# Performance work log

Hardware: AMD Instinct MI355X
Metric: run time of the kernel (lower is better)

The kernel has to match this reference:

```python
import jax, jax.numpy as jnp
import numpy as np
import math

OUT = 7   # output_size
SR = 2    # sampling_ratio


def _roi_align(feat, rois5, scale):
    """torchvision roi_align (aligned=False) for all rois against one FPN level.
    feat: [B,C,H,W], rois5: [N,5] = (batch_idx, x1, y1, x2, y2). Returns [N,C,OUT,OUT]."""
    B, C, H, W = feat.shape
    b = rois5[:, 0].astype(jnp.int32)
    x1 = rois5[:, 1] * scale
    y1 = rois5[:, 2] * scale
    x2 = rois5[:, 3] * scale
    y2 = rois5[:, 4] * scale
    rw = jnp.maximum(x2 - x1, 1.0)
    rh = jnp.maximum(y2 - y1, 1.0)
    gh = OUT * SR  # sampling grid: ph*SR+iy, sample at (g+0.5)*bin/SR from roi start
    gw = OUT * SR
    ys = y1[:, None] + (jnp.arange(gh, dtype=feat.dtype) + 0.5)[None, :] * (rh / gh)[:, None]  # [N,gh]
    xs = x1[:, None] + (jnp.arange(gw, dtype=feat.dtype) + 0.5)[None, :] * (rw / gw)[:, None]  # [N,gw]
    # torchvision bilinear_interpolate: out-of-range (< -1 or > size) -> 0, else clamp
    vy = (ys >= -1.0) & (ys <= H)
    vx = (xs >= -1.0) & (xs <= W)
    y = jnp.clip(ys, 0.0, H - 1)
    x = jnp.clip(xs, 0.0, W - 1)
    y0f = jnp.floor(y)
    x0f = jnp.floor(x)
    y0 = y0f.astype(jnp.int32)
    x0 = x0f.astype(jnp.int32)
    y1i = jnp.minimum(y0 + 1, H - 1)
    x1i = jnp.minimum(x0 + 1, W - 1)
    ly = y - y0f; hy = 1.0 - ly
    lx = x - x0f; hx = 1.0 - lx
    fT = jnp.transpose(feat, (0, 2, 3, 1))  # [B,H,W,C]

    def gather(yi, xi):
        return fT[b[:, None, None], yi[:, :, None], xi[:, None, :]]  # [N,gh,gw,C]

    w00 = (hy[:, :, None] * hx[:, None, :])[..., None]
    w01 = (hy[:, :, None] * lx[:, None, :])[..., None]
    w10 = (ly[:, :, None] * hx[:, None, :])[..., None]
    w11 = (ly[:, :, None] * lx[:, None, :])[..., None]
    val = (gather(y0, x0) * w00 + gather(y0, x1i) * w01
           + gather(y1i, x0) * w10 + gather(y1i, x1i) * w11)
    val = val * (vy[:, :, None] & vx[:, None, :])[..., None].astype(feat.dtype)
    # average SRxSR samples per output bin -> [N,OUT,OUT,C] -> [N,C,OUT,OUT]
    val = val.reshape(val.shape[0], OUT, SR, OUT, SR, C).mean(axis=(2, 4))
    return jnp.transpose(val, (0, 3, 1, 2))


def setup_inputs() -> dict:
    key = jax.random.key(0)
    ks = jax.random.split(key, 6)
    feat0 = jax.random.normal(ks[0], (2, 256, 200, 200), jnp.float32)
    feat1 = jax.random.normal(ks[1], (2, 256, 100, 100), jnp.float32)
    feat2 = jax.random.normal(ks[2], (2, 256, 50, 50), jnp.float32)
    feat3 = jax.random.normal(ks[3], (2, 256, 25, 25), jnp.float32)
    B, N = 2, 512
    xy1 = jax.random.uniform(ks[4], (B, N, 2), jnp.float32, 0.0, 700.0)
    wh = jax.random.uniform(ks[5], (B, N, 2), jnp.float32, 16.0, 320.0)
    xy2 = jnp.minimum(xy1 + wh, 799.0)
    rois = jnp.concatenate([xy1, xy2], axis=-1)  # [B,N,4] = (x1,y1,x2,y2)
    return {"feat0": feat0, "feat1": feat1, "feat2": feat2, "feat3": feat3,
            "rois": rois, "image_h": 800, "image_w": 800}


def reference(feat0, feat1, feat2, feat3, rois, image_h, image_w):
    feats = [feat0, feat1, feat2, feat3]
    B, N = rois.shape[:2]
    # _convert_to_roi_format: prepend batch index column
    bcol = jnp.repeat(jnp.arange(B, dtype=rois.dtype), N)[:, None]
    rois5 = jnp.concatenate([bcol, rois.reshape(-1, 4)], axis=1)  # [B*N,5]
    # _setup_scales / _get_scales: pow-2-rounded ratio of feature H to image H (static)
    scales = [2.0 ** round(math.log2(f.shape[2] / float(image_h))) for f in feats]
    lvl_min = -math.log2(scales[0])   # 2
    lvl_max = -math.log2(scales[-1])  # 5
    # FPN level routing: k = floor(4 + log2(sqrt(area)/224)), clamped
    area = (rois5[:, 4] - rois5[:, 2]) * (rois5[:, 3] - rois5[:, 1])
    k = jnp.floor(4.0 + jnp.log2(jnp.sqrt(area) / 224.0))
    k = jnp.clip(k, lvl_min, lvl_max) - lvl_min  # in {0,1,2,3}
    out = jnp.zeros((B * N, feats[0].shape[1], OUT, OUT), feats[0].dtype)
    for lvl, (f, s) in enumerate(zip(feats, scales)):
        pooled = _roi_align(f, rois5, s)
        out = jnp.where((k == lvl)[:, None, None, None], pooled, out)
    return out
```

## Files before the change

### kernel.cpp

```cpp
#include <hip/hip_runtime.h>

#define OUTS 7
#define SR 2
#define GRIDW 14
#define NS 196
#define NCH 256
#define NROI 1024
#define NBIN 49

#define L0_OFF 0
#define L1_OFF 20480000
#define L2_OFF 25600000
#define L3_OFF 26880000
#define WS_ELEMS 27200000

static __device__ __forceinline__ unsigned short f2bf(float f) {
    unsigned u = __builtin_bit_cast(unsigned, f);
    u += 0x7fffu + ((u >> 16) & 1u);
    return (unsigned short)(u >> 16);
}

static __device__ __forceinline__ float bfhi(unsigned u) {
    return __builtin_bit_cast(float, u & 0xffff0000u);
}
static __device__ __forceinline__ float bflo(unsigned u) {
    return __builtin_bit_cast(float, u << 16);
}

__global__ __launch_bounds__(256) void nchw_to_nhwc_bf16(
    const float* __restrict__ f0, const float* __restrict__ f1,
    const float* __restrict__ f2, const float* __restrict__ f3,
    unsigned short* __restrict__ ws) {
    __shared__ unsigned short tile[32 * 256];
    int bid = blockIdx.x;
    const float* in; unsigned short* outp; int P, ptiles, local;
    if (bid < 2500)      { in = f0; outp = ws + L0_OFF; P = 40000; ptiles = 1250; local = bid; }
    else if (bid < 3126) { in = f1; outp = ws + L1_OFF; P = 10000; ptiles = 313;  local = bid - 2500; }
    else if (bid < 3284) { in = f2; outp = ws + L2_OFF; P = 2500;  ptiles = 79;   local = bid - 3126; }
    else                 { in = f3; outp = ws + L3_OFF; P = 625;   ptiles = 20;   local = bid - 3284; }
    int pt = local % ptiles;
    int b  = local / ptiles;
    int p0 = pt * 32;
    int t = threadIdx.x;

    const float* inb = in + (size_t)b * NCH * P;
    unsigned short* outb = outp + (size_t)b * P * NCH;

    int px = (t & 7) * 4;
    int cl = t >> 3;
#pragma unroll
    for (int i = 0; i < 8; ++i) {
        int c = cl + i * 32;
        const float* src = inb + (size_t)c * P + p0 + px;
        float v[4];
        if (p0 + px + 3 < P) {
            float4 f = *(const float4*)src;
            v[0] = f.x; v[1] = f.y; v[2] = f.z; v[3] = f.w;
        } else {
#pragma unroll
            for (int k2 = 0; k2 < 4; ++k2)
                v[k2] = (p0 + px + k2 < P) ? src[k2] : 0.0f;
        }
#pragma unroll
        for (int j = 0; j < 4; ++j) {
            int p = px + j;
            int pos = ((c >> 3) ^ p) & 31;
            tile[p * 256 + pos * 8 + (c & 7)] = f2bf(v[j]);
        }
    }
    __syncthreads();

    int p = t >> 3;
    int gp = p0 + p;
    if (gp < P) {
        unsigned short* dst = outb + (size_t)gp * NCH;
#pragma unroll
        for (int it = 0; it < 4; ++it) {
            int k = (t & 7) + it * 8;
            int pos = (k ^ p) & 31;
            uint4 val = *(const uint4*)&tile[p * 256 + pos * 8];
            *(uint4*)(dst + k * 8) = val;
        }
    }
}

__global__ __launch_bounds__(256) void roi_gather_nhwc(
    const unsigned short* __restrict__ nhwc,
    const float* __restrict__ rois,
    float* __restrict__ out) {
    __shared__ int   s_off[4][NS];
    __shared__ float s_w[4][NS];
    __shared__ float lds_out[64 * 53];

    int n = blockIdx.x >> 2;
    int q = blockIdx.x & 3;
    int tid = threadIdx.x;
    int b = n >> 9;

    float x1 = rois[n * 4 + 0];
    float y1 = rois[n * 4 + 1];
    float x2 = rois[n * 4 + 2];
    float y2 = rois[n * 4 + 3];
    float area = (y2 - y1) * (x2 - x1);
    float kf = floorf(4.0f + log2f(sqrtf(area) / 224.0f));
    kf = fminf(fmaxf(kf, 2.0f), 5.0f);
    int lvl = (int)kf - 2;
    float scale = ldexpf(0.25f, -lvl);
    int H, W; size_t base;
    switch (lvl) {
        case 0:  H = 200; W = 200; base = L0_OFF; break;
        case 1:  H = 100; W = 100; base = L1_OFF; break;
        case 2:  H = 50;  W = 50;  base = L2_OFF; break;
        default: H = 25;  W = 25;  base = L3_OFF; break;
    }
    float x1s = x1 * scale, y1s = y1 * scale;
    float rw = fmaxf(x2 * scale - x1s, 1.0f);
    float rh = fmaxf(y2 * scale - y1s, 1.0f);
    float sx = rw * (1.0f / GRIDW);
    float sy = rh * (1.0f / GRIDW);

    if (tid < NS) {
        int gy = tid / GRIDW, gx = tid % GRIDW;
        float y = y1s + ((float)gy + 0.5f) * sy;
        float x = x1s + ((float)gx + 0.5f) * sx;
        bool valid = (y >= -1.0f) && (y <= (float)H) && (x >= -1.0f) && (x <= (float)W);
        float yc = fminf(fmaxf(y, 0.0f), (float)(H - 1));
        float xc = fminf(fmaxf(x, 0.0f), (float)(W - 1));
        int y0 = (int)floorf(yc), x0 = (int)floorf(xc);
        int y1i = min(y0 + 1, H - 1), x1i = min(x0 + 1, W - 1);
        float ly = yc - (float)y0, lx = xc - (float)x0;
        float hy = 1.0f - ly, hx = 1.0f - lx;
        float vm = valid ? 1.0f : 0.0f;
        s_off[0][tid] = (y0 * W + x0) * NCH;
        s_off[1][tid] = (y0 * W + x1i) * NCH;
        s_off[2][tid] = (y1i * W + x0) * NCH;
        s_off[3][tid] = (y1i * W + x1i) * NCH;
        s_w[0][tid] = hy * hx * vm;
        s_w[1][tid] = hy * lx * vm;
        s_w[2][tid] = ly * hx * vm;
        s_w[3][tid] = ly * lx * vm;
    }
    __syncthreads();

    int lane = tid & 63;
    int wave = tid >> 6;
    int t = lane >> 4;
    int j = lane & 15;
    const unsigned short* fcq =
        nhwc + base + (size_t)b * (size_t)H * W * NCH + q * 64 + j * 4;

    for (int bin = wave; bin < NBIN; bin += 4) {
        int ph = bin / OUTS, pw = bin - ph * OUTS;
        int sbase = (ph * SR) * GRIDW + pw * SR;
        float4 acc = make_float4(0.f, 0.f, 0.f, 0.f);
#pragma unroll
        for (int k = 0; k < 4; ++k) {
            int s = sbase + (k >> 1) * GRIDW + (k & 1);
            float wgt = s_w[t][s];
            uint2 v = *(const uint2*)(fcq + s_off[t][s]);
            acc.x += wgt * bflo(v.x);
            acc.y += wgt * bfhi(v.x);
            acc.z += wgt * bflo(v.y);
            acc.w += wgt * bfhi(v.y);
        }
        acc.x += __shfl_xor(acc.x, 16, 64);
        acc.y += __shfl_xor(acc.y, 16, 64);
        acc.z += __shfl_xor(acc.z, 16, 64);
        acc.w += __shfl_xor(acc.w, 16, 64);
        acc.x += __shfl_xor(acc.x, 32, 64);
        acc.y += __shfl_xor(acc.y, 32, 64);
        acc.z += __shfl_xor(acc.z, 32, 64);
        acc.w += __shfl_xor(acc.w, 32, 64);
        if (t == 0) {
            lds_out[(4 * j + 0) * 53 + bin] = acc.x * 0.25f;
            lds_out[(4 * j + 1) * 53 + bin] = acc.y * 0.25f;
            lds_out[(4 * j + 2) * 53 + bin] = acc.z * 0.25f;
            lds_out[(4 * j + 3) * 53 + bin] = acc.w * 0.25f;
        }
    }
    __syncthreads();

    float* og = out + (size_t)n * (NCH * NBIN) + (size_t)q * 64 * NBIN;
    for (int i = tid; i < 64 * NBIN; i += 256) {
        int c = i / NBIN;
        int bin = i - c * NBIN;
        og[i] = lds_out[c * 53 + bin];
    }
}


struct RoiMeta {
    float x1, y1, sx, sy;
    int level, b, pad0, pad1;
};

__global__ void prep_rois_kernel(const float* __restrict__ rois,
                                 RoiMeta* __restrict__ meta, int total) {
    int n = blockIdx.x * blockDim.x + threadIdx.x;
    if (n >= total) return;
    float x1 = rois[n * 4 + 0];
    float y1 = rois[n * 4 + 1];
    float x2 = rois[n * 4 + 2];
    float y2 = rois[n * 4 + 3];
    float area = (y2 - y1) * (x2 - x1);
    float k = floorf(4.0f + log2f(sqrtf(area) / 224.0f));
    k = fminf(fmaxf(k, 2.0f), 5.0f);
    int lvl = (int)k - 2;
    float scale = ldexpf(0.25f, -lvl);
    float x1s = x1 * scale;
    float y1s = y1 * scale;
    float rw = fmaxf(x2 * scale - x1s, 1.0f);
    float rh = fmaxf(y2 * scale - y1s, 1.0f);
    RoiMeta m;
    m.x1 = x1s; m.y1 = y1s;
    m.sx = rw / (float)(OUTS * SR);
    m.sy = rh / (float)(OUTS * SR);
    m.level = lvl;
    m.b = n / 512;
    m.pad0 = 0; m.pad1 = 0;
    meta[n] = m;
}

__global__ __launch_bounds__(256) void roi_align_kernel(
    const float* __restrict__ f0, const float* __restrict__ f1,
    const float* __restrict__ f2, const float* __restrict__ f3,
    const RoiMeta* __restrict__ meta, float* __restrict__ out, int total) {
    int idx = blockIdx.x * 256 + threadIdx.x;
    if (idx >= total) return;
    int pw = idx % OUTS;
    int ph = (idx / OUTS) % OUTS;
    int c  = (idx / (OUTS * OUTS)) & (NCH - 1);
    int n  = idx / (OUTS * OUTS * NCH);

    RoiMeta m = meta[n];
    const float* f; int H, W;
    switch (m.level) {
        case 0:  f = f0; H = 200; W = 200; break;
        case 1:  f = f1; H = 100; W = 100; break;
        case 2:  f = f2; H = 50;  W = 50;  break;
        default: f = f3; H = 25;  W = 25;  break;
    }
    const float* fc = f + (size_t)(m.b * NCH + c) * H * W;

    float acc = 0.0f;
#pragma unroll
    for (int iy = 0; iy < SR; ++iy) {
        float y = m.y1 + ((float)(ph * SR + iy) + 0.5f) * m.sy;
        if (y < -1.0f || y > (float)H) continue;
        float yc = fminf(fmaxf(y, 0.0f), (float)(H - 1));
        int y0 = (int)floorf(yc);
        int y1i = min(y0 + 1, H - 1);
        float ly = yc - (float)y0;
        float hy = 1.0f - ly;
        const float* r0 = fc + (size_t)y0 * W;
        const float* r1 = fc + (size_t)y1i * W;
#pragma unroll
        for (int ix = 0; ix < SR; ++ix) {
            float x = m.x1 + ((float)(pw * SR + ix) + 0.5f) * m.sx;
            if (x < -1.0f || x > (float)W) continue;
            float xc = fminf(fmaxf(x, 0.0f), (float)(W - 1));
            int x0 = (int)floorf(xc);
            int x1i = min(x0 + 1, W - 1);
            float lx = xc - (float)x0;
            float hx = 1.0f - lx;
            acc += hy * (hx * r0[x0] + lx * r0[x1i]) +
                   ly * (hx * r1[x0] + lx * r1[x1i]);
        }
    }
    out[idx] = acc * 0.25f;
}


extern "C" void kernel_launch(void* const* d_in, const int* in_sizes, int n_in,
                              void* d_out, int out_size, void* d_ws, size_t ws_size,
                              hipStream_t stream) {
    const float* f0 = (const float*)d_in[0];
    const float* f1 = (const float*)d_in[1];
    const float* f2 = (const float*)d_in[2];
    const float* f3 = (const float*)d_in[3];
    const float* rois = (const float*)d_in[4];
    float* out = (float*)d_out;

    if (ws_size >= (size_t)WS_ELEMS * sizeof(unsigned short)) {
        unsigned short* nhwc = (unsigned short*)d_ws;
        nchw_to_nhwc_bf16<<<3324, 256, 0, stream>>>(f0, f1, f2, f3, nhwc);
        roi_gather_nhwc<<<NROI * 4, 256, 0, stream>>>(nhwc, rois, out);
    } else {
        RoiMeta* meta = (RoiMeta*)d_ws;
        prep_rois_kernel<<<(NROI + 255) / 256, 256, 0, stream>>>(rois, meta, NROI);
        const int total = NROI * NCH * OUTS * OUTS;
        roi_align_kernel<<<(total + 255) / 256, 256, 0, stream>>>(
            f0, f1, f2, f3, meta, out, total);
    }
}
```

Measured before the change: 68.36 us.

## Retile NCHW-to-NHWC bf16 transpose as 16-channel by 1024-pixel tiles

The layout-conversion kernel now gives each block 16 channels by 1024 pixels instead of 256 channels by 32 pixels. Each block reads long contiguous pixel runs per channel and writes 32-byte channel chunks per pixel, with a padded LDS stride in place of the XOR swizzle. The block count drops from 3324 to 1728. Output writes become 32-byte segments strided by 512 bytes, which may coalesce worse than the previous full 512-byte rows, so the gain on reads may be offset.

```diff
diff --git a/kernel.cpp b/kernel.cpp
--- a/kernel.cpp
+++ b/kernel.cpp
@@ -14,6 +14,8 @@
 #define L3_OFF 26880000
 #define WS_ELEMS 27200000
 
+#define TSTRIDE 1032
+
 static __device__ __forceinline__ unsigned short f2bf(float f) {
     unsigned u = __builtin_bit_cast(unsigned, f);
     u += 0x7fffu + ((u >> 16) & 1u);
@@ -31,55 +33,65 @@
     const float* __restrict__ f0, const float* __restrict__ f1,
     const float* __restrict__ f2, const float* __restrict__ f3,
     unsigned short* __restrict__ ws) {
-    __shared__ unsigned short tile[32 * 256];
+    __shared__ unsigned short tile[16 * TSTRIDE];
     int bid = blockIdx.x;
     const float* in; unsigned short* outp; int P, ptiles, local;
-    if (bid < 2500)      { in = f0; outp = ws + L0_OFF; P = 40000; ptiles = 1250; local = bid; }
-    else if (bid < 3126) { in = f1; outp = ws + L1_OFF; P = 10000; ptiles = 313;  local = bid - 2500; }
-    else if (bid < 3284) { in = f2; outp = ws + L2_OFF; P = 2500;  ptiles = 79;   local = bid - 3126; }
-    else                 { in = f3; outp = ws + L3_OFF; P = 625;   ptiles = 20;   local = bid - 3284; }
-    int pt = local % ptiles;
-    int b  = local / ptiles;
-    int p0 = pt * 32;
+    if (bid < 1280)      { in = f0; outp = ws + L0_OFF; P = 40000; ptiles = 40; local = bid; }
+    else if (bid < 1600) { in = f1; outp = ws + L1_OFF; P = 10000; ptiles = 10; local = bid - 1280; }
+    else if (bid < 1696) { in = f2; outp = ws + L2_OFF; P = 2500;  ptiles = 3;  local = bid - 1600; }
+    else                 { in = f3; outp = ws + L3_OFF; P = 625;   ptiles = 1;  local = bid - 1696; }
+    int ct = local & 15;
+    int rest = local >> 4;
+    int pt = rest % ptiles;
+    int b  = rest / ptiles;
+    int p0 = pt * 1024;
     int t = threadIdx.x;
 
-    const float* inb = in + (size_t)b * NCH * P;
-    unsigned short* outb = outp + (size_t)b * P * NCH;
-
-    int px = (t & 7) * 4;
-    int cl = t >> 3;
-#pragma unroll
-    for (int i = 0; i < 8; ++i) {
-        int c = cl + i * 32;
-        const float* src = inb + (size_t)c * P + p0 + px;
-        float v[4];
-        if (p0 + px + 3 < P) {
-            float4 f = *(const float4*)src;
-            v[0] = f.x; v[1] = f.y; v[2] = f.z; v[3] = f.w;
-        } else {
-#pragma unroll
-            for (int k2 = 0; k2 < 4; ++k2)
-                v[k2] = (p0 + px + k2 < P) ? src[k2] : 0.0f;
-        }
-#pragma unroll
-        for (int j = 0; j < 4; ++j) {
-            int p = px + j;
-            int pos = ((c >> 3) ^ p) & 31;
-            tile[p * 256 + pos * 8 + (c & 7)] = f2bf(v[j]);
+    const float* inb = in + (size_t)(b * NCH + ct * 16) * P + p0;
+    unsigned short* outb = outp + (size_t)b * P * NCH + ct * 16;
+
+    {
+        int c = t >> 4;
+        int k4 = t & 15;
+        const float* src = inb + (size_t)c * P;
+        unsigned short* trow = &tile[c * TSTRIDE];
+        bool vec_ok = ((P & 3) == 0);
+#pragma unroll
+        for (int it = 0; it < 16; ++it) {
+            int px = (k4 + it * 16) * 4;
+            unsigned short pk[4];
+            if (vec_ok && (p0 + px + 3 < P)) {
+                float4 v = *(const float4*)(src + px);
+                pk[0] = f2bf(v.x); pk[1] = f2bf(v.y);
+                pk[2] = f2bf(v.z); pk[3] = f2bf(v.w);
+            } else {
+#pragma unroll
+                for (int k = 0; k < 4; ++k)
+                    pk[k] = (p0 + px + k < P) ? f2bf(src[px + k]) : (unsigned short)0;
+            }
+            uint2 u;
+            u.x = (unsigned)pk[0] | ((unsigned)pk[1] << 16);
+            u.y = (unsigned)pk[2] | ((unsigned)pk[3] << 16);
+            *(uint2*)&trow[px] = u;
         }
     }
     __syncthreads();
 
-    int p = t >> 3;
-    int gp = p0 + p;
-    if (gp < P) {
-        unsigned short* dst = outb + (size_t)gp * NCH;
-#pragma unroll
-        for (int it = 0; it < 4; ++it) {
-            int k = (t & 7) + it * 8;
-            int pos = (k ^ p) & 31;
-            uint4 val = *(const uint4*)&tile[p * 256 + pos * 8];
-            *(uint4*)(dst + k * 8) = val;
+#pragma unroll
+    for (int it = 0; it < 4; ++it) {
+        int p = t + it * 256;
+        int gp = p0 + p;
+        if (gp < P) {
+            unsigned pk[8];
+#pragma unroll
+            for (int m = 0; m < 8; ++m) {
+                unsigned lo = tile[(2 * m) * TSTRIDE + p];
+                unsigned hi = tile[(2 * m + 1) * TSTRIDE + p];
+                pk[m] = lo | (hi << 16);
+            }
+            unsigned short* dst = outb + (size_t)gp * NCH;
+            *(uint4*)dst       = make_uint4(pk[0], pk[1], pk[2], pk[3]);
+            *(uint4*)(dst + 8) = make_uint4(pk[4], pk[5], pk[6], pk[7]);
         }
     }
 }
@@ -283,7 +295,7 @@
 
     if (ws_size >= (size_t)WS_ELEMS * sizeof(unsigned short)) {
         unsigned short* nhwc = (unsigned short*)d_ws;
-        nchw_to_nhwc_bf16<<<3324, 256, 0, stream>>>(f0, f1, f2, f3, nhwc);
+        nchw_to_nhwc_bf16<<<1728, 256, 0, stream>>>(f0, f1, f2, f3, nhwc);
         roi_gather_nhwc<<<NROI * 4, 256, 0, stream>>>(nhwc, rois, out);
     } else {
         RoiMeta* meta = (RoiMeta*)d_ws;
```

Measured after the change: 81.58 us. 1.19x slower.
